# Kernel tuning notes

Measured on AMD Instinct MI355X. Metric: run time of the kernel, lower is better.

## Reference

```python
import jax, jax.numpy as jnp
import numpy as np

# ---- config (mirrors cfg / init kwargs) ----
FEAT_STRIDE = 16
IM_DIMS = (1024, 1024)          # (height, width)
ANCHOR_SCALES = (8, 16, 32)
ANCHOR_RATIOS = (0.5, 1.0, 2.0)
PRE_NMS_TOPN = 6000             # eval mode (cfg_key=1)
POST_NMS_TOPN = 300
NMS_THRESH = 0.7
MIN_SIZE = 16


def _generate_base_anchors(base_size=16, ratios=ANCHOR_RATIOS, scales=ANCHOR_SCALES):
    """py-faster-rcnn generate_anchors, in numpy (static)."""
    def mk(ws, hs, xc, yc):
        return np.stack([xc - 0.5 * (ws - 1), yc - 0.5 * (hs - 1),
                         xc + 0.5 * (ws - 1), yc + 0.5 * (hs - 1)], axis=1)
    base = np.array([0, 0, base_size - 1, base_size - 1], dtype=np.float64)
    w = base[2] - base[0] + 1; h = base[3] - base[1] + 1
    xc = base[0] + 0.5 * (w - 1); yc = base[1] + 0.5 * (h - 1)
    # ratio enum
    size = w * h
    ws = np.round(np.sqrt(size / np.array(ratios)))
    hs = np.round(ws * np.array(ratios))
    ratio_anchors = mk(ws, hs, xc, yc)
    # scale enum
    out = []
    for a in ratio_anchors:
        aw = a[2] - a[0] + 1; ah = a[3] - a[1] + 1
        axc = a[0] + 0.5 * (aw - 1); ayc = a[1] + 0.5 * (ah - 1)
        out.append(mk(aw * np.array(scales), ah * np.array(scales), axc, ayc))
    return np.concatenate(out, axis=0).astype(np.float32)  # [A,4]


def _all_anchors(H, W):
    base = _generate_base_anchors()                       # [A,4]
    sx = np.arange(W) * FEAT_STRIDE
    sy = np.arange(H) * FEAT_STRIDE
    sx, sy = np.meshgrid(sx, sy)
    shifts = np.stack([sx.ravel(), sy.ravel(), sx.ravel(), sy.ravel()], axis=1)  # [H*W,4]
    anchors = shifts[:, None, :].astype(np.float32) + base[None, :, :]
    return anchors.reshape(-1, 4)                         # [H*W*A, 4]


def setup_inputs() -> dict:
    key = jax.random.key(0)
    k1, k2 = jax.random.split(key)
    H, W, A = 64, 64, 9
    rpn_cls_score = jax.random.normal(k1, (1, H, W, 2 * A), dtype=jnp.float32)
    rpn_bbox_pred = jax.random.normal(k2, (1, H, W, 4 * A), dtype=jnp.float32)
    return {"rpn_cls_score": rpn_cls_score, "rpn_bbox_pred": rpn_bbox_pred}


def _proposals(rpn_cls_score, rpn_bbox_pred):
    _, H, W, C2 = rpn_cls_score.shape
    A = C2 // 2
    # rpn_softmax: per-anchor 2-way softmax, foreground prob
    scores = jax.nn.softmax(rpn_cls_score.reshape(H, W, A, 2), axis=-1)[..., 1].reshape(-1)  # [N]
    deltas = rpn_bbox_pred.reshape(-1, 4)                  # [N,4]
    anchors = jnp.asarray(_all_anchors(H, W))              # [N,4]
    # bbox_transform_inv
    aw = anchors[:, 2] - anchors[:, 0] + 1.0
    ah = anchors[:, 3] - anchors[:, 1] + 1.0
    axc = anchors[:, 0] + 0.5 * aw
    ayc = anchors[:, 1] + 0.5 * ah
    dx, dy, dw, dh = deltas[:, 0], deltas[:, 1], deltas[:, 2], deltas[:, 3]
    pxc = dx * aw + axc; pyc = dy * ah + ayc
    pw = jnp.exp(dw) * aw; ph = jnp.exp(dh) * ah
    x1 = pxc - 0.5 * pw; y1 = pyc - 0.5 * ph
    x2 = pxc + 0.5 * pw; y2 = pyc + 0.5 * ph
    # clip to image
    im_h, im_w = IM_DIMS
    x1 = jnp.clip(x1, 0.0, im_w - 1.0); x2 = jnp.clip(x2, 0.0, im_w - 1.0)
    y1 = jnp.clip(y1, 0.0, im_h - 1.0); y2 = jnp.clip(y2, 0.0, im_h - 1.0)
    boxes = jnp.stack([x1, y1, x2, y2], axis=1)            # [N,4]
    # filter too-small boxes by masking their score
    valid = ((x2 - x1 + 1.0) >= MIN_SIZE) & ((y2 - y1 + 1.0) >= MIN_SIZE)
    scores = jnp.where(valid, scores, -jnp.inf)
    return boxes, scores


def _nms_keep(boxes, K):
    """Greedy NMS keep-mask over score-descending boxes [K,4]."""
    x1, y1, x2, y2 = boxes[:, 0], boxes[:, 1], boxes[:, 2], boxes[:, 3]
    areas = (x2 - x1 + 1.0) * (y2 - y1 + 1.0)
    ix1 = jnp.maximum(x1[:, None], x1[None, :])
    iy1 = jnp.maximum(y1[:, None], y1[None, :])
    ix2 = jnp.minimum(x2[:, None], x2[None, :])
    iy2 = jnp.minimum(y2[:, None], y2[None, :])
    iw = jnp.maximum(ix2 - ix1 + 1.0, 0.0)
    ih = jnp.maximum(iy2 - iy1 + 1.0, 0.0)
    inter = iw * ih
    iou = inter / (areas[:, None] + areas[None, :] - inter)  # [K,K]
    idxs = jnp.arange(K)
    def body(i, keep):
        sup = keep[i] & (iou[i] > NMS_THRESH) & (idxs > i)
        return keep & ~sup
    return jax.lax.fori_loop(0, K, body, jnp.ones((K,), bool))


def reference(rpn_cls_score, rpn_bbox_pred):
    boxes, scores = _proposals(rpn_cls_score, rpn_bbox_pred)
    K = min(PRE_NMS_TOPN, scores.shape[0])
    top_scores, order = jax.lax.top_k(scores, K)           # score-descending
    top_boxes = boxes[order]                               # [K,4]
    keep = _nms_keep(top_boxes, K)
    sel_scores = jnp.where(keep, top_scores, -jnp.inf)
    _, idx = jax.lax.top_k(sel_scores, POST_NMS_TOPN)      # kept, in score order
    out_boxes = top_boxes[idx]                             # [post,4]
    blob = jnp.concatenate([jnp.zeros((POST_NMS_TOPN, 1), out_boxes.dtype), out_boxes], axis=1)
    return blob                                            # [post,5] (batch_idx, x1,y1,x2,y2)
```

## Files before the change

kernel.cpp:

```cpp
#include <hip/hip_runtime.h>
#include <stdint.h>

typedef unsigned long long u64;
typedef unsigned int u32;

#define N_ANCH 36864
#define WGRID 64
#define A_PER 9
#define KTOP 6000
#define NOUT 300
#define NBIN 5120
#define NCHK 94
#define NJ   6016
#define NSLOT 12
#define SPILLCAP 64

#define BARRIER_LDS() do {                                   \
    asm volatile("s_waitcnt lgkmcnt(0)" ::: "memory");       \
    __builtin_amdgcn_s_barrier();                            \
    asm volatile("" ::: "memory");                           \
} while (0)

__constant__ float c_ax1[9] = {-84.f,-176.f,-360.f,-56.f,-120.f,-248.f,-36.f,-80.f,-168.f};
__constant__ float c_ay1[9] = {-40.f,-88.f,-184.f,-56.f,-120.f,-248.f,-80.f,-168.f,-344.f};
__constant__ float c_aw[9]  = {184.f,368.f,736.f,128.f,256.f,512.f,88.f,176.f,352.f};
__constant__ float c_ah[9]  = {96.f,192.f,384.f,128.f,256.f,512.f,176.f,352.f,704.f};

__device__ __forceinline__ u32 binof(u32 u) {
    if (u < 0x80000000u) return 0u;
    if (u < 0xBF000000u) return 1u + ((u - 0x80000000u) >> 22);
    return 256u + ((u - 0xBF000000u) >> 11);
}

__device__ __forceinline__ bool iou_gt(float4 a, float areaA, float4 b, float areaB) {
    float ix1 = fmaxf(a.x, b.x), iy1 = fmaxf(a.y, b.y);
    float ix2 = fminf(a.z, b.z), iy2 = fminf(a.w, b.w);
    float iw = fmaxf(ix2 - ix1 + 1.0f, 0.0f);
    float ih = fmaxf(iy2 - iy1 + 1.0f, 0.0f);
    float inter = iw * ih;
    float iou = inter / (areaA + areaB - inter);
    return iou > 0.7f;
}

__global__ __launch_bounds__(256) void proposal_kernel(const float* __restrict__ cls,
                                                       const float* __restrict__ dlt,
                                                       u64* __restrict__ keys,
                                                       float4* __restrict__ boxes,
                                                       u32* __restrict__ hist) {
    __shared__ u32 lh[NBIN];
    const int t = threadIdx.x;
    const int lane = t & 63;
    for (int b = t; b < NBIN; b += 256) lh[b] = 0;
    __syncthreads();

    int i = blockIdx.x * 256 + t;
    int a  = i % A_PER;
    int hw = i / A_PER;
    int wx = hw % WGRID;
    int hy = hw / WGRID;

    float2 lp = *(const float2*)(cls + hw * 18 + 2 * a);
    float l0 = lp.x, l1 = lp.y;
    float m  = fmaxf(l0, l1);
    float e0 = expf(l0 - m), e1 = expf(l1 - m);
    float s  = e1 / (e0 + e1);

    float4 dd = *(const float4*)(dlt + hw * 36 + 4 * a);
    float dx = dd.x, dy = dd.y, dw = dd.z, dh = dd.w;
    float aw = c_aw[a], ah = c_ah[a];
    float axc = (c_ax1[a] + 16.f * (float)wx) + 0.5f * aw;
    float ayc = (c_ay1[a] + 16.f * (float)hy) + 0.5f * ah;

    float pxc = dx * aw + axc;
    float pyc = dy * ah + ayc;
    float pw  = expf(dw) * aw;
    float phh = expf(dh) * ah;
    float x1 = pxc - 0.5f * pw, y1 = pyc - 0.5f * phh;
    float x2 = pxc + 0.5f * pw, y2 = pyc + 0.5f * phh;
    x1 = fminf(fmaxf(x1, 0.f), 1023.f);
    x2 = fminf(fmaxf(x2, 0.f), 1023.f);
    y1 = fminf(fmaxf(y1, 0.f), 1023.f);
    y2 = fminf(fmaxf(y2, 0.f), 1023.f);
    bool valid = ((x2 - x1 + 1.f) >= 16.f) && ((y2 - y1 + 1.f) >= 16.f);
    float sc = valid ? s : -__builtin_huge_valf();

    u32 sb  = __float_as_uint(sc);
    u32 ord = (sb & 0x80000000u) ? ~sb : (sb | 0x80000000u);
    u64 key = ((u64)ord << 32) | (u32)(~(u32)i);
    keys[i]  = key;
    boxes[i] = make_float4(x1, y1, x2, y2);

    u64 infb = __ballot(!valid);
    if (valid) {
        atomicAdd(&lh[binof(ord)], 1u);
    } else {
        if (lane == __builtin_ctzll(infb))
            atomicAdd(&lh[0], (u32)__popcll(infb));
    }
    __syncthreads();
    for (int b = t; b < NBIN; b += 256) {
        u32 x = lh[b];
        if (x) atomicAdd(&hist[b], x);
    }
}

__global__ __launch_bounds__(256) void scan_kernel(const u32* __restrict__ hist,
                                                   u32* __restrict__ binStart,
                                                   u32* __restrict__ gEV) {
    __shared__ u32 wsum[4];
    const int t = threadIdx.x;
    const int lane = t & 63;
    const int v = t >> 6;
    if (t == 0) gEV[1] = KTOP;
    int hi = NBIN - 1 - (NBIN / 256) * t;
    u32 cnt[NBIN / 256];
    u32 sum = 0;
#pragma unroll
    for (int k = 0; k < NBIN / 256; ++k) { cnt[k] = hist[hi - k]; sum += cnt[k]; }
    u32 s = sum;
#pragma unroll
    for (int d = 1; d < 64; d <<= 1) {
        u32 x = __shfl_up(s, d, 64);
        if (lane >= d) s += x;
    }
    if (lane == 63) wsum[v] = s;
    __syncthreads();
    u32 base = 0;
#pragma unroll
    for (int q = 0; q < 4; ++q) { u32 x = wsum[q]; if (q < v) base += x; }
    u32 run = base + s - sum;
#pragma unroll
    for (int k = 0; k < NBIN / 256; ++k) {
        int b = hi - k;
        binStart[b] = run;
        u32 end = run + cnt[k];
        if (run < KTOP && end >= KTOP) gEV[0] = end;
        run = end;
    }
}

__global__ __launch_bounds__(256) void scatter_kernel(const u64* __restrict__ keys,
                                                      const u32* __restrict__ binStart,
                                                      u32* __restrict__ cursor,
                                                      u64* __restrict__ scat) {
    int i = blockIdx.x * 256 + threadIdx.x;
    u64 k = keys[i];
    u32 b = binof((u32)(k >> 32));
    u32 s0 = binStart[b];
    if (s0 < KTOP) {
        u32 p = s0 + atomicAdd(&cursor[b], 1u);
        scat[p] = k;
    }
}

__global__ __launch_bounds__(256) void rank_kernel(const u64* __restrict__ scat,
                                                   const u32* __restrict__ binStart,
                                                   const u32* __restrict__ hist,
                                                   const float4* __restrict__ boxes,
                                                   u32* __restrict__ gEV,
                                                   float4* __restrict__ topBoxes) {
    int i = blockIdx.x * 256 + threadIdx.x;
    u32 E = gEV[0];
    if (i >= (int)E) return;
    u64 k = scat[i];
    u32 b = binof((u32)(k >> 32));
    u32 s0 = binStart[b], c = hist[b];
    u32 r = s0;
    for (u32 j = s0; j < s0 + c; ++j) r += (scat[j] > k) ? 1u : 0u;
    if (r < KTOP) {
        int idx = (int)(~(u32)k);
        topBoxes[r] = boxes[idx];
        if (!(k >> 63)) atomicMin((int*)&gEV[1], (int)r);
    }
}

__global__ __launch_bounds__(256) void maskT_kernel(const float4* __restrict__ topBoxes,
                                                    const u32* __restrict__ gEV,
                                                    u64* __restrict__ S) {
    const int V = (int)gEV[1];
    const int nch = (V + 63) >> 6;
    const int ntask = nch * (nch + 1) / 2;
    const int lane = threadIdx.x & 63;
    const int v = threadIdx.x >> 6;
    for (int tk = blockIdx.x * 4 + v; tk < ntask; tk += gridDim.x * 4) {
        int jc = (int)((sqrtf(8.f * (float)tk + 1.f) - 1.f) * 0.5f);
        while ((jc + 1) * (jc + 2) / 2 <= tk) ++jc;
        while (jc * (jc + 1) / 2 > tk) --jc;
        int w = tk - jc * (jc + 1) / 2;
        int ci = w * 64 + lane;
        float4 bi = (ci < V) ? topBoxes[ci] : make_float4(0.f, 0.f, -8.f, -8.f);
        float ai = (bi.z - bi.x + 1.f) * (bi.w - bi.y + 1.f);
        int j = jc * 64 + lane;
        float4 bj = (j < V) ? topBoxes[j] : make_float4(0.f, 0.f, -8.f, -8.f);
        float aj = (bj.z - bj.x + 1.f) * (bj.w - bj.y + 1.f);
        u64 m = 0;
#pragma unroll 4
        for (int b = 0; b < 64; ++b) {
            float4 bb;
            bb.x = __shfl(bi.x, b, 64); bb.y = __shfl(bi.y, b, 64);
            bb.z = __shfl(bi.z, b, 64); bb.w = __shfl(bi.w, b, 64);
            float ab = __shfl(ai, b, 64);
            if (iou_gt(bb, ab, bj, aj)) m |= (1ull << b);
        }
        if (w == jc) m &= ((1ull << lane) - 1ull);
        S[(u64)w * NJ + j] = m;
    }
}

#define SLOT_DECL(K) u64 kw##K = 0, pa##K = 0, pb##K = 0; u32 ao##K = 0;
#define SLOT_ACC(K)  if (nslot > 4*(K) + v) { accA |= pa##K & kw##K; accB |= pb##K & kw##K; }
#define SLOT_REF(K)  if (nslot > 4*(K) + v) { const u64* rp_ = S + (u64)ao##K * NJ + ofsn; pa##K = rp_[0]; pb##K = rp_[64]; }
#define SLOT_CASE(K) case K: kw##K = kb_; ao##K = wch_; if (pf_) { const u64* rp_ = S + (u64)wch_ * NJ + onx_; pa##K = rp_[0]; pb##K = rp_[64]; } break;
#define DO_CLAIM(KB, WCH) do {                                                \
    u64 kb_ = (KB); u32 wch_ = (WCH);                                         \
    int si_ = nslot >> 2, so_ = nslot & 3;                                    \
    if (si_ < NSLOT) {                                                        \
      if (v == so_) {                                                         \
        bool pf_ = (r + 1 < nr);                                              \
        u64 onx_ = (u64)(128 * (r + 1)) + lane;                               \
        switch (si_) {                                                        \
          SLOT_CASE(0) SLOT_CASE(1) SLOT_CASE(2) SLOT_CASE(3)                 \
          SLOT_CASE(4) SLOT_CASE(5) SLOT_CASE(6) SLOT_CASE(7)                 \
          SLOT_CASE(8) SLOT_CASE(9) SLOT_CASE(10) SLOT_CASE(11)               \
          default: break;                                                     \
        }                                                                     \
      }                                                                       \
      ++nslot;                                                                \
    } else if (nspill < SPILLCAP) {                                           \
      if (v == 3 && lane == 0) { spillW[nspill] = wch_; spillK[nspill] = kb_; } \
      ++nspill; sadd = true;                                                  \
    }                                                                         \
  } while (0)

__global__ __launch_bounds__(256, 1) void nms_out_kernel(const float4* __restrict__ topBoxes,
                                                         const u32* __restrict__ gEV,
                                                         const u64* __restrict__ S,
                                                         float* __restrict__ out) {
    __shared__ u64 keepw[NCHK];
    __shared__ u64 supw[2][8];
    __shared__ u64 spillK[SPILLCAP];
    __shared__ u32 spillW[SPILLCAP];
    __shared__ u32 wsum[4];
    const int t = threadIdx.x;
    const int lane = t & 63;
    const int v = t >> 6;
    const int V = (int)gEV[1];
    const int nch = (V + 63) >> 6;
    const int nr  = (nch + 1) >> 1;
    if (t < NCHK) keepw[t] = 0;

    SLOT_DECL(0) SLOT_DECL(1) SLOT_DECL(2) SLOT_DECL(3)
    SLOT_DECL(4) SLOT_DECL(5) SLOT_DECL(6) SLOT_DECL(7)
    SLOT_DECL(8) SLOT_DECL(9) SLOT_DECL(10) SLOT_DECL(11)

    u64 dAc  = S[lane];
    u64 dABc = S[64 + lane];
    u64 dBc  = S[(u64)NJ + 64 + lane];
    int nslot = 0, nspill = 0, nkept = 0;

    for (int r = 0; r < nr; ++r) {
        const int par = r & 1;
        u64 accA = 0, accB = 0;
        SLOT_ACC(0) SLOT_ACC(1) SLOT_ACC(2) SLOT_ACC(3)
        SLOT_ACC(4) SLOT_ACC(5) SLOT_ACC(6) SLOT_ACC(7)
        SLOT_ACC(8) SLOT_ACC(9) SLOT_ACC(10) SLOT_ACC(11)
        for (int s2 = v; s2 < nspill; s2 += 4) {
            u64 kk = spillK[s2];
            const u64* row = S + (u64)spillW[s2] * NJ + 128 * r + lane;
            accA |= row[0] & kk; accB |= row[64] & kk;
        }
        u64 bA = __ballot(accA != 0ull), bB = __ballot(accB != 0ull);
        if (lane == 0) { supw[par][v] = bA; supw[par][4 + v] = bB; }
        u64 dAn = 0, dABn = 0, dBn = 0;
        if (r + 1 < nr) {
            u64 ofsn = (u64)(128 * (r + 1)) + lane;
            SLOT_REF(0) SLOT_REF(1) SLOT_REF(2) SLOT_REF(3)
            SLOT_REF(4) SLOT_REF(5) SLOT_REF(6) SLOT_REF(7)
            SLOT_REF(8) SLOT_REF(9) SLOT_REF(10) SLOT_REF(11)
            int rn = r + 1;
            dAn  = S[(u64)(2 * rn) * NJ + 128 * rn + lane];
            dABn = S[(u64)(2 * rn) * NJ + 128 * rn + 64 + lane];
            dBn  = S[(u64)(2 * rn + 1) * NJ + 128 * rn + 64 + lane];
        }
        BARRIER_LDS();
        u64 rwA = supw[par][0] | supw[par][1] | supw[par][2] | supw[par][3];
        u64 rwB = supw[par][4] | supw[par][5] | supw[par][6] | supw[par][7];
        int remA = V - 128 * r;
        int remB = remA - 64;
        u64 aliveA = (remA >= 64) ? ~0ull : ((remA <= 0) ? 0ull : ((1ull << remA) - 1ull));
        u64 aliveB = (remB >= 64) ? ~0ull : ((remB <= 0) ? 0ull : ((1ull << remB) - 1ull));
        u64 candA = ~rwA & aliveA, kbA = 0;
        while (candA) {
            int b = __builtin_ctzll(candA);
            kbA |= (1ull << b);
            candA &= ~(1ull << b);
            candA &= ~__ballot(((dAc >> b) & 1ull) != 0ull);
        }
        u64 supAB = __ballot((dABc & kbA) != 0ull);
        u64 candB = ~(rwB | supAB) & aliveB, kbB = 0;
        while (candB) {
            int b = __builtin_ctzll(candB);
            kbB |= (1ull << b);
            candB &= ~(1ull << b);
            candB &= ~__ballot(((dBc >> b) & 1ull) != 0ull);
        }
        if (t == 0) { keepw[2 * r] = kbA; if (2 * r + 1 < nch) keepw[2 * r + 1] = kbB; }
        bool sadd = false;
        if (kbA) DO_CLAIM(kbA, (u32)(2 * r));
        if (kbB) DO_CLAIM(kbB, (u32)(2 * r + 1));
        if (sadd) BARRIER_LDS();
        nkept += __popcll(kbA) + __popcll(kbB);
        dAc = dAn; dABc = dABn; dBc = dBn;
        if (nkept >= NOUT) break;
    }
    __syncthreads();

    const int per = 24;
    int r0 = t * per;
    int r1 = min(r0 + per, KTOP);
    u32 cnt2 = 0;
    for (int rr = r0; rr < r1; ++rr)
        cnt2 += (u32)((keepw[rr >> 6] >> (rr & 63)) & 1ull);
    u32 s2 = cnt2;
#pragma unroll
    for (int d = 1; d < 64; d <<= 1) {
        u32 x = __shfl_up(s2, d, 64);
        if (lane >= d) s2 += x;
    }
    if (lane == 63) wsum[v] = s2;
    __syncthreads();
    u32 base = 0, total = 0;
#pragma unroll
    for (int q = 0; q < 4; ++q) {
        u32 x = wsum[q];
        if (q < v) base += x;
        total += x;
    }
    const int n1 = min((int)total, NOUT);
    int kp = (int)(base + s2 - cnt2);
    for (int rr = r0; rr < r1; ++rr) {
        int kept = (int)((keepw[rr >> 6] >> (rr & 63)) & 1ull);
        int pos = kept ? kp : (n1 + rr - kp);
        if (pos < NOUT) {
            float4 b = topBoxes[rr];
            out[pos * 5 + 0] = 0.f;
            out[pos * 5 + 1] = b.x; out[pos * 5 + 2] = b.y;
            out[pos * 5 + 3] = b.z; out[pos * 5 + 4] = b.w;
        }
        kp += kept;
    }
}

extern "C" void kernel_launch(void* const* d_in, const int* in_sizes, int n_in,
                              void* d_out, int out_size, void* d_ws, size_t ws_size,
                              hipStream_t stream) {
    const float* cls = (const float*)d_in[0];
    const float* dlt = (const float*)d_in[1];
    float* out = (float*)d_out;
    char* ws = (char*)d_ws;
    u64*    keys     = (u64*)   (ws);
    u64*    scat     = (u64*)   (ws + 294912);
    float4* boxes    = (float4*)(ws + 589824);
    float4* topBoxes = (float4*)(ws + 1179648);
    u32*    hist     = (u32*)   (ws + 1275648);
    u32*    cursor   = (u32*)   (ws + 1296128);
    u32*    binStart = (u32*)   (ws + 1316608);
    u32*    gEV      = (u32*)   (ws + 1337088);
    u64*    S        = (u64*)   (ws + 1337344);

    hipMemsetAsync(hist, 0, 2 * NBIN * sizeof(u32), stream);
    proposal_kernel<<<144, 256, 0, stream>>>(cls, dlt, keys, boxes, hist);
    scan_kernel<<<1, 256, 0, stream>>>(hist, binStart, gEV);
    scatter_kernel<<<144, 256, 0, stream>>>(keys, binStart, cursor, scat);
    rank_kernel<<<144, 256, 0, stream>>>(scat, binStart, hist, boxes, gEV, topBoxes);
    maskT_kernel<<<1120, 256, 0, stream>>>(topBoxes, gEV, S);
    nms_out_kernel<<<1, 256, 0, stream>>>(topBoxes, gEV, S, out);
}
```

Before: 114.8 us.

## Fuse histogram, scan, scatter and rank into one single-block select kernel

The global histogram, bin scan, scatter and rank kernels and the memset are replaced by one 1024-thread kernel. It builds the histogram in LDS, scans it, scatters candidate keys into an LDS buffer (spilling to global past 6144 entries) and ranks them to pick the top boxes. This removes four kernel launches, the memset and the global atomics. In exchange, the whole 36864-key pass and the O(bin-size) ranking loop now run on a single workgroup, which gives up the parallelism of the 144-block grid.

```diff
diff --git a/kernel.cpp b/kernel.cpp
--- a/kernel.cpp
+++ b/kernel.cpp
@@ -14,6 +14,7 @@
 #define NJ   6016
 #define NSLOT 12
 #define SPILLCAP 64
+#define SCAP 6144
 
 #define BARRIER_LDS() do {                                   \
     asm volatile("s_waitcnt lgkmcnt(0)" ::: "memory");       \
@@ -45,14 +46,8 @@
 __global__ __launch_bounds__(256) void proposal_kernel(const float* __restrict__ cls,
                                                        const float* __restrict__ dlt,
                                                        u64* __restrict__ keys,
-                                                       float4* __restrict__ boxes,
-                                                       u32* __restrict__ hist) {
-    __shared__ u32 lh[NBIN];
+                                                       float4* __restrict__ boxes) {
     const int t = threadIdx.x;
-    const int lane = t & 63;
-    for (int b = t; b < NBIN; b += 256) lh[b] = 0;
-    __syncthreads();
-
     int i = blockIdx.x * 256 + t;
     int a  = i % A_PER;
     int hw = i / A_PER;
@@ -89,34 +84,35 @@
     u64 key = ((u64)ord << 32) | (u32)(~(u32)i);
     keys[i]  = key;
     boxes[i] = make_float4(x1, y1, x2, y2);
-
-    u64 infb = __ballot(!valid);
-    if (valid) {
-        atomicAdd(&lh[binof(ord)], 1u);
-    } else {
-        if (lane == __builtin_ctzll(infb))
-            atomicAdd(&lh[0], (u32)__popcll(infb));
-    }
-    __syncthreads();
-    for (int b = t; b < NBIN; b += 256) {
-        u32 x = lh[b];
-        if (x) atomicAdd(&hist[b], x);
-    }
-}
-
-__global__ __launch_bounds__(256) void scan_kernel(const u32* __restrict__ hist,
-                                                   u32* __restrict__ binStart,
-                                                   u32* __restrict__ gEV) {
-    __shared__ u32 wsum[4];
+}
+
+__global__ __launch_bounds__(1024) void select_kernel(const u64* __restrict__ keys,
+                                                      const float4* __restrict__ boxes,
+                                                      u64* __restrict__ gscat,
+                                                      float4* __restrict__ topBoxes,
+                                                      u32* __restrict__ gEV) {
+    __shared__ u32 lh[NBIN];
+    __shared__ u32 bst[NBIN];
+    __shared__ u64 scat[SCAP];
+    __shared__ u32 wsum[16];
+    __shared__ int sE;
+    __shared__ int sV;
     const int t = threadIdx.x;
     const int lane = t & 63;
     const int v = t >> 6;
-    if (t == 0) gEV[1] = KTOP;
-    int hi = NBIN - 1 - (NBIN / 256) * t;
-    u32 cnt[NBIN / 256];
+    for (int b = t; b < NBIN; b += 1024) lh[b] = 0;
+    if (t == 0) { sV = KTOP; sE = KTOP; }
+    __syncthreads();
+    for (int i = t; i < N_ANCH; i += 1024) {
+        u32 hiw = (u32)(keys[i] >> 32);
+        atomicAdd(&lh[binof(hiw)], 1u);
+    }
+    __syncthreads();
+    int hi = NBIN - 1 - 5 * t;
+    u32 cnt[5];
     u32 sum = 0;
 #pragma unroll
-    for (int k = 0; k < NBIN / 256; ++k) { cnt[k] = hist[hi - k]; sum += cnt[k]; }
+    for (int k = 0; k < 5; ++k) { cnt[k] = lh[hi - k]; sum += cnt[k]; }
     u32 s = sum;
 #pragma unroll
     for (int d = 1; d < 64; d <<= 1) {
@@ -127,51 +123,47 @@
     __syncthreads();
     u32 base = 0;
 #pragma unroll
-    for (int q = 0; q < 4; ++q) { u32 x = wsum[q]; if (q < v) base += x; }
+    for (int q = 0; q < 16; ++q) { u32 x = wsum[q]; if (q < v) base += x; }
     u32 run = base + s - sum;
 #pragma unroll
-    for (int k = 0; k < NBIN / 256; ++k) {
+    for (int k = 0; k < 5; ++k) {
         int b = hi - k;
-        binStart[b] = run;
+        bst[b] = run;
+        lh[b] = 0;
         u32 end = run + cnt[k];
-        if (run < KTOP && end >= KTOP) gEV[0] = end;
+        if (run < KTOP && end >= KTOP) sE = (int)end;
         run = end;
     }
-}
-
-__global__ __launch_bounds__(256) void scatter_kernel(const u64* __restrict__ keys,
-                                                      const u32* __restrict__ binStart,
-                                                      u32* __restrict__ cursor,
-                                                      u64* __restrict__ scat) {
-    int i = blockIdx.x * 256 + threadIdx.x;
-    u64 k = keys[i];
-    u32 b = binof((u32)(k >> 32));
-    u32 s0 = binStart[b];
-    if (s0 < KTOP) {
-        u32 p = s0 + atomicAdd(&cursor[b], 1u);
-        scat[p] = k;
-    }
-}
-
-__global__ __launch_bounds__(256) void rank_kernel(const u64* __restrict__ scat,
-                                                   const u32* __restrict__ binStart,
-                                                   const u32* __restrict__ hist,
-                                                   const float4* __restrict__ boxes,
-                                                   u32* __restrict__ gEV,
-                                                   float4* __restrict__ topBoxes) {
-    int i = blockIdx.x * 256 + threadIdx.x;
-    u32 E = gEV[0];
-    if (i >= (int)E) return;
-    u64 k = scat[i];
-    u32 b = binof((u32)(k >> 32));
-    u32 s0 = binStart[b], c = hist[b];
-    u32 r = s0;
-    for (u32 j = s0; j < s0 + c; ++j) r += (scat[j] > k) ? 1u : 0u;
-    if (r < KTOP) {
-        int idx = (int)(~(u32)k);
-        topBoxes[r] = boxes[idx];
-        if (!(k >> 63)) atomicMin((int*)&gEV[1], (int)r);
-    }
+    __syncthreads();
+    for (int i = t; i < N_ANCH; i += 1024) {
+        u64 k = keys[i];
+        u32 b = binof((u32)(k >> 32));
+        u32 s0 = bst[b];
+        if (s0 < KTOP) {
+            u32 p = s0 + atomicAdd(&lh[b], 1u);
+            if (p < SCAP) scat[p] = k; else gscat[p] = k;
+        }
+    }
+    __syncthreads();
+    const int E = sE;
+    for (int i = t; i < E; i += 1024) {
+        u64 k = (i < SCAP) ? scat[i] : gscat[i];
+        u32 b = binof((u32)(k >> 32));
+        u32 s0 = bst[b];
+        u32 e0 = (b > 0) ? bst[b - 1] : (u32)N_ANCH;
+        u32 r = s0;
+        for (u32 j = s0; j < e0; ++j) {
+            u64 kj = (j < SCAP) ? scat[j] : gscat[j];
+            r += (kj > k) ? 1u : 0u;
+        }
+        if (r < KTOP) {
+            int idx = (int)(~(u32)k);
+            topBoxes[r] = boxes[idx];
+            if (!(k >> 63)) atomicMin(&sV, (int)r);
+        }
+    }
+    __syncthreads();
+    if (t == 0) gEV[1] = (u32)sV;
 }
 
 __global__ __launch_bounds__(256) void maskT_kernel(const float4* __restrict__ topBoxes,
@@ -359,20 +351,14 @@
     float* out = (float*)d_out;
     char* ws = (char*)d_ws;
     u64*    keys     = (u64*)   (ws);
-    u64*    scat     = (u64*)   (ws + 294912);
+    u64*    gscat    = (u64*)   (ws + 294912);
     float4* boxes    = (float4*)(ws + 589824);
     float4* topBoxes = (float4*)(ws + 1179648);
-    u32*    hist     = (u32*)   (ws + 1275648);
-    u32*    cursor   = (u32*)   (ws + 1296128);
-    u32*    binStart = (u32*)   (ws + 1316608);
     u32*    gEV      = (u32*)   (ws + 1337088);
     u64*    S        = (u64*)   (ws + 1337344);
 
-    hipMemsetAsync(hist, 0, 2 * NBIN * sizeof(u32), stream);
-    proposal_kernel<<<144, 256, 0, stream>>>(cls, dlt, keys, boxes, hist);
-    scan_kernel<<<1, 256, 0, stream>>>(hist, binStart, gEV);
-    scatter_kernel<<<144, 256, 0, stream>>>(keys, binStart, cursor, scat);
-    rank_kernel<<<144, 256, 0, stream>>>(scat, binStart, hist, boxes, gEV, topBoxes);
+    proposal_kernel<<<144, 256, 0, stream>>>(cls, dlt, keys, boxes);
+    select_kernel<<<1, 1024, 0, stream>>>(keys, boxes, gscat, topBoxes, gEV);
     maskT_kernel<<<1120, 256, 0, stream>>>(topBoxes, gEV, S);
     nms_out_kernel<<<1, 256, 0, stream>>>(topBoxes, gEV, S, out);
 }
```

Result: slower. 136.7 us (+19.1%).
